# Optimization experiments

Hardware: AMD Instinct MI355X
Metric: run time of the kernel (lower is better)

## Reference

```python
import jax, jax.numpy as jnp
import numpy as np

RES = 14          # window resolution -> N = RES*RES = 196
NUM_HEADS = 24
HEAD_DIM = 32
DIM = NUM_HEADS * HEAD_DIM  # 768
CPB_HIDDEN = 512
BATCH = 128


def _swin2_table_index(res):
    """Swin-v2 continuous relative position bias: log-spaced coords table
    [(2r-1)^2, 2] and relative position index [N*N] (numpy, static)."""
    r = res
    coords = np.arange(-(r - 1), r, dtype=np.float32)
    table = np.stack(np.meshgrid(coords, coords, indexing="ij"), axis=-1)  # [2r-1, 2r-1, 2]
    table = table / (r - 1)  # pretrained_window_size == window_size
    table = table * 8.0
    table = np.sign(table) * np.log2(np.abs(table) + 1.0) / np.log2(8.0)
    table = table.reshape(-1, 2)

    grid = np.stack(np.meshgrid(np.arange(r), np.arange(r), indexing="ij"))  # [2, r, r]
    grid = grid.reshape(2, -1)  # [2, N]
    rel = grid[:, :, None] - grid[:, None, :]  # [2, N, N]
    rel = rel.transpose(1, 2, 0).astype(np.int64)  # [N, N, 2]
    rel[..., 0] += r - 1
    rel[..., 1] += r - 1
    rel[..., 0] *= 2 * r - 1
    index = rel.sum(-1).reshape(-1)  # [N*N]
    return table, index


def setup_inputs() -> dict:
    key = jax.random.key(0)
    ks = jax.random.split(key, 5)
    N = RES * RES
    x = jax.random.normal(ks[0], (BATCH, N, DIM), dtype=jnp.float32)
    qkv_w = jax.random.normal(ks[1], (DIM, 3 * DIM), dtype=jnp.float32) * (DIM ** -0.5)
    qkv_b = jnp.zeros((3 * DIM,), dtype=jnp.float32)
    proj_w = jax.random.normal(ks[2], (DIM, DIM), dtype=jnp.float32) * (DIM ** -0.5)
    proj_b = jnp.zeros((DIM,), dtype=jnp.float32)
    cpb_w1 = jax.random.normal(ks[3], (2, CPB_HIDDEN), dtype=jnp.float32) * (2 ** -0.5)
    cpb_b1 = jnp.zeros((CPB_HIDDEN,), dtype=jnp.float32)
    cpb_w2 = jax.random.normal(ks[4], (CPB_HIDDEN, NUM_HEADS), dtype=jnp.float32) * (CPB_HIDDEN ** -0.5)
    cpb_b2 = jnp.zeros((NUM_HEADS,), dtype=jnp.float32)
    return {"x": x, "qkv_w": qkv_w, "qkv_b": qkv_b, "proj_w": proj_w,
            "proj_b": proj_b, "cpb_w1": cpb_w1, "cpb_b1": cpb_b1,
            "cpb_w2": cpb_w2, "cpb_b2": cpb_b2}


def reference(x, qkv_w, qkv_b, proj_w, proj_b, cpb_w1, cpb_b1, cpb_w2, cpb_b2):
    B, N, C = x.shape
    H, hd = NUM_HEADS, HEAD_DIM

    table_np, index_np = _swin2_table_index(RES)
    table = jnp.asarray(table_np)            # [(2r-1)^2, 2]
    index = jnp.asarray(index_np)            # [N*N] int

    # qkv projection -> (3, B, H, N, hd)
    qkv = x @ qkv_w + qkv_b
    qkv = qkv.reshape(B, N, 3, H, hd).transpose(2, 0, 3, 1, 4)
    q, k, v = qkv[0], qkv[1], qkv[2]

    # scaled QK^T
    attn = jnp.einsum("bhnd,bhmd->bhnm", q, k) / jnp.sqrt(jnp.float32(hd))

    # continuous relative position bias: MLP(2->512->H), gather, 16*sigmoid
    h1 = jax.nn.relu(table @ cpb_w1 + cpb_b1)           # [(2r-1)^2, 512]
    bias_table = h1 @ cpb_w2 + cpb_b2                    # [(2r-1)^2, H]
    bias = bias_table[index].reshape(N, N, H).transpose(2, 0, 1)  # [H, N, N]
    bias = 16.0 * jax.nn.sigmoid(bias)

    attn = jax.nn.softmax(attn + bias[None], axis=-1)

    out = jnp.einsum("bhnm,bhmd->bhnd", attn, v)
    out = out.transpose(0, 2, 1, 3).reshape(B, N, C)
    out = out @ proj_w + proj_b
    return out
```

## Files before the change

### kernel.cpp

```cpp
#include <hip/hip_runtime.h>
#include <hip/hip_bf16.h>

typedef unsigned short u16;
typedef __attribute__((ext_vector_type(8))) short short8;
typedef __attribute__((ext_vector_type(4))) short short4v;
typedef __attribute__((ext_vector_type(8))) u16 u16x8;
typedef __attribute__((ext_vector_type(4))) u16 u16x4;
typedef __attribute__((ext_vector_type(4))) float f32x4;

__device__ __forceinline__ u16 f2bf(float f) {
  __hip_bfloat16 h = __float2bfloat16(f);
  u16 u;
  __builtin_memcpy(&u, &h, 2);
  return u;
}

__device__ __forceinline__ f32x4 mfma16(short8 a, short8 b, f32x4 c) {
  return __builtin_amdgcn_mfma_f32_16x16x32_bf16(a, b, c, 0, 0, 0);
}

__device__ __forceinline__ f32x4 mfma16x16(short4v a, short4v b, f32x4 c) {
#if __has_builtin(__builtin_amdgcn_mfma_f32_16x16x16bf16_1k)
  return __builtin_amdgcn_mfma_f32_16x16x16bf16_1k(a, b, c, 0, 0, 0);
#else
  asm("v_mfma_f32_16x16x16_bf16 %0, %1, %2, %0" : "+v"(c) : "v"(a), "v"(b));
  return c;
#endif
}

__device__ __forceinline__ void gl_lds16(const void* g, void* l) {
  __builtin_amdgcn_global_load_lds(
      (const __attribute__((address_space(1))) unsigned int*)g,
      (__attribute__((address_space(3))) unsigned int*)l, 16, 0, 0);
}

__global__ __launch_bounds__(256) void cvt_x_k(const float* __restrict__ x,
                                               u16* __restrict__ xb) {
  int i = (blockIdx.x * 256 + threadIdx.x) * 4;
  float4 v = *(const float4*)(x + i);
  u16x4 o = { f2bf(v.x), f2bf(v.y), f2bf(v.z), f2bf(v.w) };
  *(u16x4*)(xb + i) = o;
}

__global__ __launch_bounds__(256) void cvt_wt_k(const float* __restrict__ w,
                                                u16* __restrict__ wt, int N) {
  int i = blockIdx.x * 256 + threadIdx.x;
  int nn = i / 768, kk = i % 768;
  wt[i] = f2bf(w[(size_t)kk * N + nn]);
}

__device__ __forceinline__ float cpb_coord(int v) {
  float c = (float)(v - 13) * (8.0f / 13.0f);
  float a = fabsf(c);
  float r = log2f(a + 1.0f) * (1.0f / 3.0f);
  return c < 0.f ? -r : r;
}

__global__ __launch_bounds__(64) void bias_mlp_k(
    const float* __restrict__ w1, const float* __restrict__ b1,
    const float* __restrict__ w2, const float* __restrict__ b2,
    float* __restrict__ btab) {
  int e = blockIdx.x;
  int lane = threadIdx.x;
  float t0 = cpb_coord(e / 27), t1 = cpb_coord(e % 27);
  float acc[24];
#pragma unroll
  for (int hh = 0; hh < 24; hh++) acc[hh] = 0.f;
#pragma unroll
  for (int jj = 0; jj < 8; jj++) {
    int j = lane * 8 + jj;
    float h1 = t0 * w1[j] + t1 * w1[512 + j] + b1[j];
    h1 = fmaxf(h1, 0.f);
#pragma unroll
    for (int hh = 0; hh < 24; hh++) acc[hh] += h1 * w2[j * 24 + hh];
  }
#pragma unroll
  for (int hh = 0; hh < 24; hh++)
#pragma unroll
    for (int m = 1; m < 64; m <<= 1) acc[hh] += __shfl_xor(acc[hh], m, 64);
  if (lane == 0) {
#pragma unroll
    for (int hh = 0; hh < 24; hh++) {
      float v = acc[hh] + b2[hh];
      btab[e * 24 + hh] = 16.f / (1.f + __expf(-v));
    }
  }
}

__global__ __launch_bounds__(256) void bias_expand_k(const float* __restrict__ tab,
                                                     float* __restrict__ be) {
  int i = blockIdx.x * 256 + threadIdx.x;
  int h = i / (196 * 208);
  int rem = i % (196 * 208);
  int row = rem / 208, col = rem % 208;
  float v = 0.f;
  if (col < 196) {
    int dy = row / 14 - col / 14 + 13;
    int dx = row % 14 - col % 14 + 13;
    v = tab[(dy * 27 + dx) * 24 + h] * 1.4426950408889634f;
  }
  be[i] = v;
}

template <int EPI>
__global__ __launch_bounds__(256) void gemm_k(
    const u16* __restrict__ A, const u16* __restrict__ Bt,
    const float* __restrict__ bias, float* __restrict__ Cf,
    u16* __restrict__ Cb, int N, int K, int nbx) {
  __shared__ u16 As[128 * 64];
  __shared__ u16 Bs[128 * 64];
  const int tid = threadIdx.x, lane = tid & 63, w = tid >> 6;
  const int r16 = lane & 15, q4 = lane >> 4;
  const int wr = w >> 1, wc = w & 1;
  const int nwg = gridDim.x, cpx = nwg >> 3;
  const int swz = (blockIdx.x & 7) * cpx + (blockIdx.x >> 3);
  const int m0 = (swz / nbx) * 128, n0 = (swz % nbx) * 128;

  f32x4 acc[4][4] = {};

  for (int k0 = 0; k0 < K; k0 += 64) {
#pragma unroll
    for (int g = 0; g < 4; g++) {
      int chunk = (w * 4 + g) * 64 + lane;
      int row = chunk >> 3, p = chunk & 7;
      int gch = p ^ (row & 7);
      gl_lds16(A + (size_t)(m0 + row) * K + k0 + gch * 8, (char*)As + (w * 4 + g) * 1024);
      gl_lds16(Bt + (size_t)(n0 + row) * K + k0 + gch * 8, (char*)Bs + (w * 4 + g) * 1024);
    }
    __syncthreads();
#pragma unroll
    for (int kk = 0; kk < 2; kk++) {
      short8 af[4], bfr[4];
#pragma unroll
      for (int i = 0; i < 4; i++) {
        int row = wr * 64 + i * 16 + r16;
        int pc = (kk * 4 + q4) ^ (r16 & 7);
        af[i] = *(const short8*)((const char*)As + row * 128 + pc * 16);
      }
#pragma unroll
      for (int j = 0; j < 4; j++) {
        int row = wc * 64 + j * 16 + r16;
        int pc = (kk * 4 + q4) ^ (r16 & 7);
        bfr[j] = *(const short8*)((const char*)Bs + row * 128 + pc * 16);
      }
#pragma unroll
      for (int i = 0; i < 4; i++)
#pragma unroll
        for (int j = 0; j < 4; j++) acc[i][j] = mfma16(af[i], bfr[j], acc[i][j]);
    }
    __syncthreads();
  }

  const int nb = n0 + wc * 64 + r16;
  float bn[4];
#pragma unroll
  for (int j = 0; j < 4; j++) bn[j] = bias[nb + j * 16];
#pragma unroll
  for (int i = 0; i < 4; i++) {
#pragma unroll
    for (int r = 0; r < 4; r++) {
      int m = m0 + wr * 64 + i * 16 + q4 * 4 + r;
      if (EPI == 1) {
        float* cp = Cf + (size_t)m * N + nb;
#pragma unroll
        for (int j = 0; j < 4; j++) cp[j * 16] = acc[i][j][r] + bn[j];
      } else {
        u16* cp = Cb + (size_t)m * N + nb;
#pragma unroll
        for (int j = 0; j < 4; j++) cp[j * 16] = f2bf(acc[i][j][r] + bn[j]);
      }
    }
  }
}

__global__ __launch_bounds__(256) void attn_k(
    const u16* __restrict__ qkv, const float* __restrict__ be,
    u16* __restrict__ ao) {
  constexpr int VST = 236;
  __shared__ u16 Ks[208 * 32];
  __shared__ u16 Vt[32 * VST];
  const int tid = threadIdx.x, lane = tid & 63, w = tid >> 6;
  const int r16 = lane & 15, q4 = lane >> 4;
  const int bh = blockIdx.x, b = bh / 24, h = bh % 24;
  const u16* qp = qkv + (size_t)(b * 196) * 2304 + h * 32;
  const u16* kp = qp + 768;
  const u16* vp = qp + 1536;
  const float* bp = be + h * (196 * 208);
  const int ksw = (q4 ^ ((r16 >> 1) & 3)) * 16;
  const float SC2 = 0.17677669529663687f * 1.4426950408889634f;

  for (int g = w; g < 13; g += 4) {
    int chunk = g * 64 + lane;
    int row = chunk >> 2;
    int gch = (chunk & 3) ^ ((row >> 1) & 3);
    gl_lds16(kp + (size_t)row * 2304 + gch * 8, (char*)Ks + g * 1024);
  }
  for (int c = tid; c < 784; c += 256) {
    int n = c >> 2, d0 = (c & 3) * 8;
    u16x8 vv = *(const u16x8*)(vp + (size_t)n * 2304 + (c & 3) * 8);
#pragma unroll
    for (int jj = 0; jj < 8; jj++) Vt[(d0 + jj) * VST + n] = vv[jj];
  }
  for (int idx = tid; idx < 32 * 40; idx += 256) {
    int d = idx / 40, n = 196 + idx % 40;
    Vt[d * VST + n] = 0;
  }
  __syncthreads();

  const f32x4 z = {0.f, 0.f, 0.f, 0.f};
  short8 bq = *(const short8*)(qp + (size_t)(w * 16 + r16) * 2304 + q4 * 8);
  for (int si = w; si < 13; si += 4) {
    short8 bq_next = {};
    if (si + 4 < 13)
      bq_next = *(const short8*)(qp + (size_t)((si + 4) * 16 + r16) * 2304 + q4 * 8);
    int gc = si * 16 + r16;
    gc = gc < 196 ? gc : 195;
    const float* brow = bp + gc * 208 + q4 * 4;
    float s0 = 0.f, s1 = 0.f, s2 = 0.f, s3 = 0.f;
    short4v pa[13];
#pragma unroll
    for (int t = 0; t < 13; t++) {
      short8 ka = *(const short8*)((const char*)Ks + (t * 16 + r16) * 64 + ksw);
      f32x4 p = mfma16(ka, bq, z);
      float4 bv = *(const float4*)(brow + t * 16);
      float e0 = __builtin_amdgcn_exp2f(p[0] * SC2 + bv.x);
      float e1 = __builtin_amdgcn_exp2f(p[1] * SC2 + bv.y);
      float e2 = __builtin_amdgcn_exp2f(p[2] * SC2 + bv.z);
      float e3 = __builtin_amdgcn_exp2f(p[3] * SC2 + bv.w);
      if (t == 12) {
        int k0 = 192 + q4 * 4;
        e0 = (k0 + 0 < 196) ? e0 : 0.f;
        e1 = (k0 + 1 < 196) ? e1 : 0.f;
        e2 = (k0 + 2 < 196) ? e2 : 0.f;
        e3 = (k0 + 3 < 196) ? e3 : 0.f;
      }
      s0 += e0; s1 += e1; s2 += e2; s3 += e3;
      pa[t][0] = (short)f2bf(e0);
      pa[t][1] = (short)f2bf(e1);
      pa[t][2] = (short)f2bf(e2);
      pa[t][3] = (short)f2bf(e3);
    }
    bq = bq_next;
    float sum = (s0 + s1) + (s2 + s3);
    sum += __shfl_xor(sum, 16, 64);
    sum += __shfl_xor(sum, 32, 64);
    float rs = 1.0f / sum;
    f32x4 o0a = z, o0b = z, o1a = z, o1b = z;
    __builtin_amdgcn_s_setprio(1);
#pragma unroll
    for (int t = 0; t < 13; t++) {
      const u16* vrow = &Vt[r16 * VST + t * 16 + q4 * 4];
      short4v b0 = *(const short4v*)vrow;
      short4v b1 = *(const short4v*)(vrow + 16 * VST);
      if (t & 1) {
        o0b = mfma16x16(pa[t], b0, o0b);
        o1b = mfma16x16(pa[t], b1, o1b);
      } else {
        o0a = mfma16x16(pa[t], b0, o0a);
        o1a = mfma16x16(pa[t], b1, o1a);
      }
    }
    __builtin_amdgcn_s_setprio(0);
#pragma unroll
    for (int r = 0; r < 4; r++) {
      float rsv = __shfl(rs, q4 * 4 + r, 16);
      int grow = si * 16 + q4 * 4 + r;
      if (grow < 196) {
        u16* op = ao + ((size_t)(b * 196 + grow)) * 768 + h * 32;
        op[r16] = f2bf((o0a[r] + o0b[r]) * rsv);
        op[16 + r16] = f2bf((o1a[r] + o1b[r]) * rsv);
      }
    }
  }
}

extern "C" void kernel_launch(void* const* d_in, const int* in_sizes, int n_in,
                              void* d_out, int out_size, void* d_ws, size_t ws_size,
                              hipStream_t stream) {
  const float* x = (const float*)d_in[0];
  const float* qkv_w = (const float*)d_in[1];
  const float* qkv_b = (const float*)d_in[2];
  const float* proj_w = (const float*)d_in[3];
  const float* proj_b = (const float*)d_in[4];
  const float* cpb_w1 = (const float*)d_in[5];
  const float* cpb_b1 = (const float*)d_in[6];
  const float* cpb_w2 = (const float*)d_in[7];
  const float* cpb_b2 = (const float*)d_in[8];
  float* out = (float*)d_out;

  char* ws = (char*)d_ws;
  size_t o = 0;
  auto alloc = [&](size_t sz) {
    size_t r = o;
    o = (o + sz + 255) & ~(size_t)255;
    return r;
  };
  const size_t ME = (size_t)25088 * 768;
  u16* x_bf = (u16*)(ws + alloc(ME * 2));
  u16* wq_t = (u16*)(ws + alloc((size_t)2304 * 768 * 2));
  u16* wp_t = (u16*)(ws + alloc((size_t)768 * 768 * 2));
  u16* qkv_s = (u16*)(ws + alloc(3 * ME * 2));
  float* btab = (float*)(ws + alloc((size_t)729 * 24 * 4));
  float* bexp = (float*)(ws + alloc((size_t)24 * 196 * 208 * 4));
  u16* ao = x_bf;

  cvt_x_k<<<18816, 256, 0, stream>>>(x, x_bf);
  cvt_wt_k<<<6912, 256, 0, stream>>>(qkv_w, wq_t, 2304);
  cvt_wt_k<<<2304, 256, 0, stream>>>(proj_w, wp_t, 768);
  bias_mlp_k<<<729, 64, 0, stream>>>(cpb_w1, cpb_b1, cpb_w2, cpb_b2, btab);
  bias_expand_k<<<3822, 256, 0, stream>>>(btab, bexp);
  gemm_k<0><<<3528, 256, 0, stream>>>(x_bf, wq_t, qkv_b, nullptr, qkv_s,
                                      2304, 768, 18);
  attn_k<<<3072, 256, 0, stream>>>(qkv_s, bexp, ao);
  gemm_k<1><<<1176, 256, 0, stream>>>(ao, wp_t, proj_b, out, nullptr,
                                      768, 768, 6);
}
```

Baseline: 288.7 us.

## Use 256x256 double-buffered 8-wave GEMM for QKV projection

```diff
diff --git a/kernel.cpp b/kernel.cpp
--- a/kernel.cpp
+++ b/kernel.cpp
@@ -102,11 +102,147 @@
   be[i] = v;
 }
 
-template <int EPI>
+__global__ __launch_bounds__(512) void gemm256_k(
+    const u16* __restrict__ A, const u16* __restrict__ Bt,
+    const float* __restrict__ bias, u16* __restrict__ Cb, int N, int nbx) {
+  __shared__ u16 lds[65536];
+  char* ldsb = (char*)lds;
+  const int tid = threadIdx.x, lane = tid & 63, w = tid >> 6;
+  const int r16 = lane & 15, q4 = lane >> 4;
+  const int wm = w >> 2, wn = w & 3;
+  const int nwg = gridDim.x;
+  const int qq = nwg >> 3, rr = nwg & 7;
+  const int xcd = blockIdx.x & 7, bidx = blockIdx.x >> 3;
+  const int swz = (xcd < rr) ? xcd * (qq + 1) + bidx
+                             : rr * (qq + 1) + (xcd - rr) * qq + bidx;
+  const int m0 = (swz / nbx) * 256, n0 = (swz % nbx) * 256;
+  const u16* Ab = A + (size_t)m0 * 768;
+  const u16* Bb = Bt + (size_t)n0 * 768;
+
+  auto stage = [&](const u16* __restrict__ src, int matBase, int sdst, int h) {
+    char* base = ldsb + matBase + (sdst & 1) * 32768 + h * 16384 + w * 1024;
+    const int k0 = sdst * 64;
+#pragma unroll
+    for (int g = 0; g < 2; g++) {
+      int c = g * 512 + tid;
+      int row = c >> 3, p = c & 7;
+      int gch = p ^ (row & 7);
+      gl_lds16(src + (size_t)(h * 128 + row) * 768 + k0 + gch * 8,
+               base + g * 8192 + lane * 16);
+    }
+  };
+
+  f32x4 acc[8][4] = {};
+
+  stage(Ab, 0, 0, 0);
+  stage(Ab, 0, 0, 1);
+  stage(Bb, 65536, 0, 0);
+  stage(Bb, 65536, 0, 1);
+  stage(Ab, 0, 1, 0);
+  asm volatile("s_waitcnt vmcnt(2)" ::: "memory");
+  __builtin_amdgcn_s_barrier();
+
+  const int pcb = r16 & 7;
+  for (int s = 0; s < 12; s++) {
+    const int bA = (s & 1) * 32768;
+    const int bB = 65536 + (s & 1) * 32768;
+    short8 afr[4][2], bfr[4][2];
+#pragma unroll
+    for (int i = 0; i < 4; i++)
+#pragma unroll
+      for (int kk = 0; kk < 2; kk++)
+        afr[i][kk] = *(const short8*)(ldsb + bA +
+                         (wm * 128 + i * 16 + r16) * 128 +
+                         (((kk * 4 + q4) ^ pcb) << 4));
+#pragma unroll
+    for (int j = 0; j < 4; j++)
+#pragma unroll
+      for (int kk = 0; kk < 2; kk++)
+        bfr[j][kk] = *(const short8*)(ldsb + bB +
+                         (wn * 64 + j * 16 + r16) * 128 +
+                         (((kk * 4 + q4) ^ pcb) << 4));
+    if (s < 11) stage(Ab, 0, s + 1, 1);
+    __builtin_amdgcn_s_barrier();
+    __builtin_amdgcn_s_setprio(1);
+#pragma unroll
+    for (int kk = 0; kk < 2; kk++)
+#pragma unroll
+      for (int i = 0; i < 4; i++)
+#pragma unroll
+        for (int j = 0; j < 2; j++)
+          acc[i][j] = mfma16(afr[i][kk], bfr[j][kk], acc[i][j]);
+    __builtin_amdgcn_s_setprio(0);
+    __builtin_amdgcn_s_barrier();
+    if (s < 11) stage(Bb, 65536, s + 1, 0);
+    __builtin_amdgcn_s_barrier();
+    __builtin_amdgcn_s_setprio(1);
+#pragma unroll
+    for (int kk = 0; kk < 2; kk++)
+#pragma unroll
+      for (int i = 0; i < 4; i++)
+#pragma unroll
+        for (int j = 2; j < 4; j++)
+          acc[i][j] = mfma16(afr[i][kk], bfr[j][kk], acc[i][j]);
+    __builtin_amdgcn_s_setprio(0);
+    __builtin_amdgcn_s_barrier();
+#pragma unroll
+    for (int i = 0; i < 4; i++)
+#pragma unroll
+      for (int kk = 0; kk < 2; kk++)
+        afr[i][kk] = *(const short8*)(ldsb + bA +
+                         (wm * 128 + (4 + i) * 16 + r16) * 128 +
+                         (((kk * 4 + q4) ^ pcb) << 4));
+    if (s < 11) stage(Bb, 65536, s + 1, 1);
+    __builtin_amdgcn_s_barrier();
+    __builtin_amdgcn_s_setprio(1);
+#pragma unroll
+    for (int kk = 0; kk < 2; kk++)
+#pragma unroll
+      for (int i = 0; i < 4; i++)
+#pragma unroll
+        for (int j = 0; j < 2; j++)
+          acc[4 + i][j] = mfma16(afr[i][kk], bfr[j][kk], acc[4 + i][j]);
+    __builtin_amdgcn_s_setprio(0);
+    __builtin_amdgcn_s_barrier();
+    if (s < 10) {
+      stage(Ab, 0, s + 2, 0);
+      asm volatile("s_waitcnt vmcnt(2)" ::: "memory");
+    } else if (s == 10) {
+      asm volatile("s_waitcnt vmcnt(0)" ::: "memory");
+    }
+    __builtin_amdgcn_s_barrier();
+    __builtin_amdgcn_s_setprio(1);
+#pragma unroll
+    for (int kk = 0; kk < 2; kk++)
+#pragma unroll
+      for (int i = 0; i < 4; i++)
+#pragma unroll
+        for (int j = 2; j < 4; j++)
+          acc[4 + i][j] = mfma16(afr[i][kk], bfr[j][kk], acc[4 + i][j]);
+    __builtin_amdgcn_s_setprio(0);
+    __builtin_amdgcn_s_barrier();
+  }
+
+  const int nb = n0 + wn * 64 + r16;
+  float bn[4];
+#pragma unroll
+  for (int j = 0; j < 4; j++) bn[j] = bias[nb + j * 16];
+#pragma unroll
+  for (int mf = 0; mf < 8; mf++) {
+#pragma unroll
+    for (int r = 0; r < 4; r++) {
+      int m = m0 + wm * 128 + mf * 16 + q4 * 4 + r;
+      u16* cp = Cb + (size_t)m * N + nb;
+#pragma unroll
+      for (int j = 0; j < 4; j++) cp[j * 16] = f2bf(acc[mf][j][r] + bn[j]);
+    }
+  }
+}
+
 __global__ __launch_bounds__(256) void gemm_k(
     const u16* __restrict__ A, const u16* __restrict__ Bt,
     const float* __restrict__ bias, float* __restrict__ Cf,
-    u16* __restrict__ Cb, int N, int K, int nbx) {
+    int N, int K, int nbx) {
   __shared__ u16 As[128 * 64];
   __shared__ u16 Bs[128 * 64];
   const int tid = threadIdx.x, lane = tid & 63, w = tid >> 6;
@@ -160,15 +296,9 @@
 #pragma unroll
     for (int r = 0; r < 4; r++) {
       int m = m0 + wr * 64 + i * 16 + q4 * 4 + r;
-      if (EPI == 1) {
-        float* cp = Cf + (size_t)m * N + nb;
-#pragma unroll
-        for (int j = 0; j < 4; j++) cp[j * 16] = acc[i][j][r] + bn[j];
-      } else {
-        u16* cp = Cb + (size_t)m * N + nb;
-#pragma unroll
-        for (int j = 0; j < 4; j++) cp[j * 16] = f2bf(acc[i][j][r] + bn[j]);
-      }
+      float* cp = Cf + (size_t)m * N + nb;
+#pragma unroll
+      for (int j = 0; j < 4; j++) cp[j * 16] = acc[i][j][r] + bn[j];
     }
   }
 }
@@ -309,9 +439,7 @@
   cvt_wt_k<<<2304, 256, 0, stream>>>(proj_w, wp_t, 768);
   bias_mlp_k<<<729, 64, 0, stream>>>(cpb_w1, cpb_b1, cpb_w2, cpb_b2, btab);
   bias_expand_k<<<3822, 256, 0, stream>>>(btab, bexp);
-  gemm_k<0><<<3528, 256, 0, stream>>>(x_bf, wq_t, qkv_b, nullptr, qkv_s,
-                                      2304, 768, 18);
+  gemm256_k<<<882, 512, 0, stream>>>(x_bf, wq_t, qkv_b, qkv_s, 2304, 9);
   attn_k<<<3072, 256, 0, stream>>>(qkv_s, bexp, ao);
-  gemm_k<1><<<1176, 256, 0, stream>>>(ao, wp_t, proj_b, out, nullptr,
-                                      768, 768, 6);
-}
+  gemm_k<<<1176, 256, 0, stream>>>(ao, wp_t, proj_b, out, 768, 768, 6);
+}
```

Measured after the change: 283.9 us. No clear change (-1.7%).
